# Performance work log

Hardware: AMD Instinct MI355X
Metric: run time of the kernel (lower is better)

The kernel has to match this reference:

```python
import jax, jax.numpy as jnp
import numpy as np

B, L, H, E = 4, 2048, 16, 64  # batch, seq, heads, head_dim (S=L, D=E)


def setup_inputs() -> dict:
    key = jax.random.key(0)
    kq, kk, kv = jax.random.split(key, 3)
    queries = jax.random.normal(kq, (B, L, H, E), dtype=jnp.float32)
    keys = jax.random.normal(kk, (B, L, H, E), dtype=jnp.float32)
    values = jax.random.normal(kv, (B, L, H, E), dtype=jnp.float32)
    return {"queries": queries, "keys": keys, "values": values}


def reference(queries, keys, values):
    Bq, Lq, Hq, Eq = queries.shape
    scale = 1.0 / float(np.sqrt(Eq))
    # scores: [B, H, L, S]
    scores = jnp.einsum('blhe,bshe->bhls', queries, keys)
    # causal mask: forbid attending to future positions (strict upper triangle)
    causal = jnp.triu(jnp.ones((Lq, Lq), dtype=bool), k=1)
    scores = jnp.where(causal[None, None, :, :], -jnp.inf, scores)
    A = jax.nn.softmax(scale * scores, axis=-1)  # dropout p=0 -> identity
    V = jnp.einsum('bhls,bshd->blhd', A, values)  # [B, L, H, D]
    return V
```

## Files before the change

### kernel.cpp

```cpp
#include <hip/hip_runtime.h>
#include <hip/hip_bf16.h>

typedef short bs8 __attribute__((ext_vector_type(8)));
typedef short bs4 __attribute__((ext_vector_type(4)));
typedef float f32x4 __attribute__((ext_vector_type(4)));
typedef float f32x16 __attribute__((ext_vector_type(16)));
typedef int i32x4 __attribute__((ext_vector_type(4)));

#define B_ 4
#define L_ 2048
#define H_ 16
#define E_ 64
#define KT_ 64
#define KSTR 72
#define SCSTR 68
#define NEG_INF (-1e30f)
#define SCALE_LOG2E (0.125f * 1.44269504088896340736f)

__device__ __forceinline__ short bf16of(float x) {
  __hip_bfloat16 h = __float2bfloat16(x);
  return *reinterpret_cast<short*>(&h);
}

__global__ __launch_bounds__(256) void prep(const float* __restrict__ K,
                                            const float* __restrict__ V,
                                            short* __restrict__ Kb,
                                            short* __restrict__ Vt) {
  __shared__ unsigned int lt[64 * 35];
  const int tid = threadIdx.x;
  if (blockIdx.x < 1024) {
    size_t base = (size_t)blockIdx.x * 256 + tid;
#pragma unroll
    for (int i = 0; i < 8; ++i) {
      size_t g = base + (size_t)i * 262144;
      int e4 = g & 15;
      int h  = (g >> 4) & 15;
      int s  = (g >> 8) & 2047;
      int b  = (int)(g >> 19);
      float4 v = *(const float4*)(K + g * 4);
      bs4 o;
      o.x = bf16of(v.x); o.y = bf16of(v.y); o.z = bf16of(v.z); o.w = bf16of(v.w);
      *(bs4*)(Kb + (((size_t)(b * 16 + h) * L_ + s) * E_ + e4 * 4)) = o;
    }
  } else {
    int vb = blockIdx.x - 1024;
    int st = vb & 31, bh = vb >> 5;
    int b = bh >> 4, h = bh & 15;
    int s0 = st * 64;
#pragma unroll
    for (int i = 0; i < 2; ++i) {
      int idx = i * 256 + tid;
      int sp = idx >> 4;
      int e4 = idx & 15;
      const float* p0 = V + (((size_t)b * L_ + s0 + 2 * sp) * H_ + h) * E_ + e4 * 4;
      float4 v0 = *(const float4*)p0;
      float4 v1 = *(const float4*)(p0 + H_ * E_);
      unsigned u;
      u = (unsigned short)bf16of(v0.x) | ((unsigned)(unsigned short)bf16of(v1.x) << 16);
      lt[(e4 * 4 + 0) * 35 + sp] = u;
      u = (unsigned short)bf16of(v0.y) | ((unsigned)(unsigned short)bf16of(v1.y) << 16);
      lt[(e4 * 4 + 1) * 35 + sp] = u;
      u = (unsigned short)bf16of(v0.z) | ((unsigned)(unsigned short)bf16of(v1.z) << 16);
      lt[(e4 * 4 + 2) * 35 + sp] = u;
      u = (unsigned short)bf16of(v0.w) | ((unsigned)(unsigned short)bf16of(v1.w) << 16);
      lt[(e4 * 4 + 3) * 35 + sp] = u;
    }
    __syncthreads();
#pragma unroll
    for (int i = 0; i < 2; ++i) {
      int idx = i * 256 + tid;
      int e  = idx >> 3;
      int s8 = idx & 7;
      uint4 o;
      o.x = lt[e * 35 + s8 * 4 + 0];
      o.y = lt[e * 35 + s8 * 4 + 1];
      o.z = lt[e * 35 + s8 * 4 + 2];
      o.w = lt[e * 35 + s8 * 4 + 3];
      *(uint4*)(Vt + ((size_t)bh * E_ + e) * L_ + s0 + 8 * s8) = o;
    }
  }
}

__global__ __launch_bounds__(256, 4) void flash_fwd(const float* __restrict__ Q,
                                                    const short* __restrict__ Kb,
                                                    const short* __restrict__ Vt,
                                                    float* __restrict__ O) {
  const int id  = blockIdx.x;
  const int xcd = id & 7;
  const int j   = id >> 3;
  const int bh  = xcd * 8 + (j >> 4);
  const int p   = j & 15;
  const int b = bh >> 4, h = bh & 15;
  const int tid = threadIdx.x;
  const int w = tid >> 6;
  const int g = w >> 1;
  const int s = w & 1;
  const int lane = tid & 63;
  const int l32 = lane & 31;
  const int hh  = lane >> 5;
  const int h8  = hh * 8;

  __shared__ __align__(16) char smem[18432];
  short* ldsK = (short*)smem;
  short* ldsV = (short*)(smem + KT_ * KSTR * 2);
  float* scb  = (float*)smem;

  const short* KbBase = Kb + (size_t)bh * L_ * E_;
  const short* VtBase = Vt + (size_t)bh * E_ * L_;

  const int sr = tid >> 3;
  const int sc8 = (tid & 7) * 8;

  for (int phase = 0; phase < 2; ++phase) {
    const int qt  = phase ? (31 - p) : p;
    const int q0w = qt * 64 + 32 * s;
    const int nkt = qt + 1;

    bs8 aQ[4];
    {
      const float* qp = Q + (((size_t)b * L_ + q0w + l32) * H_ + h) * E_ + h8;
#pragma unroll
      for (int ks = 0; ks < 4; ++ks) {
        float4 f0 = *(const float4*)(qp + ks * 16);
        float4 f1 = *(const float4*)(qp + ks * 16 + 4);
        bs8 a;
        a[0] = bf16of(f0.x * SCALE_LOG2E); a[1] = bf16of(f0.y * SCALE_LOG2E);
        a[2] = bf16of(f0.z * SCALE_LOG2E); a[3] = bf16of(f0.w * SCALE_LOG2E);
        a[4] = bf16of(f1.x * SCALE_LOG2E); a[5] = bf16of(f1.y * SCALE_LOG2E);
        a[6] = bf16of(f1.z * SCALE_LOG2E); a[7] = bf16of(f1.w * SCALE_LOG2E);
        aQ[ks] = a;
      }
    }

    f32x16 accO[2];
#pragma unroll
    for (int d = 0; d < 2; ++d)
#pragma unroll
      for (int r = 0; r < 16; ++r) accO[d][r] = 0.f;
    float accL = 0.f;

    bs8 pfK[2], pfV[2];
#pragma unroll
    for (int i = 0; i < 2; ++i) {
      pfK[i] = *(const bs8*)(KbBase + (size_t)(sr + 32 * i) * E_ + sc8);
      pfV[i] = *(const bs8*)(VtBase + (size_t)(sr + 32 * i) * L_ + sc8);
    }

    for (int kt = 0; kt < nkt; ++kt) {
      const int k0 = kt * KT_;
      __syncthreads();
#pragma unroll
      for (int i = 0; i < 2; ++i) {
        *(bs8*)&ldsK[(sr + 32 * i) * KSTR + sc8] = pfK[i];
        *(bs8*)&ldsV[(sr + 32 * i) * KSTR + sc8] = pfV[i];
      }
      if (kt + 1 < nkt) {
        const int kn = k0 + KT_;
#pragma unroll
        for (int i = 0; i < 2; ++i) {
          pfK[i] = *(const bs8*)(KbBase + (size_t)(kn + sr + 32 * i) * E_ + sc8);
          pfV[i] = *(const bs8*)(VtBase + (size_t)(sr + 32 * i) * L_ + kn + sc8);
        }
      }
      __syncthreads();

      const int kb = k0 + 32 * g;
      if (kb <= q0w + 31) {
        const bool diag = (kb + 31 > q0w);

        f32x16 cc;
#pragma unroll
        for (int r = 0; r < 16; ++r) cc[r] = 0.f;
#pragma unroll
        for (int ks = 0; ks < 4; ++ks) {
          bs8 aK = *(const bs8*)&ldsK[(32 * g + l32) * KSTR + ks * 16 + h8];
          cc = __builtin_amdgcn_mfma_f32_32x32x16_bf16(aK, aQ[ks], cc, 0, 0, 0);
        }
        if (diag) {
          const int qcol = q0w + l32;
#pragma unroll
          for (int r = 0; r < 16; ++r) {
            const int key = kb + ((r & 3) + 8 * (r >> 2) + 4 * hh);
            if (key > qcol) cc[r] = NEG_INF;
          }
        }
        float pv[16];
#pragma unroll
        for (int r = 0; r < 16; ++r) pv[r] = exp2f(cc[r]);
        accL += ((((pv[0] + pv[1]) + (pv[2] + pv[3])) + ((pv[4] + pv[5]) + (pv[6] + pv[7]))) +
                 (((pv[8] + pv[9]) + (pv[10] + pv[11])) + ((pv[12] + pv[13]) + (pv[14] + pv[15]))));
        unsigned pk[8];
#pragma unroll
        for (int i = 0; i < 8; ++i)
          pk[i] = (unsigned)(unsigned short)bf16of(pv[2 * i]) |
                  ((unsigned)(unsigned short)bf16of(pv[2 * i + 1]) << 16);
        unsigned w0 = pk[0], w2 = pk[2];
        asm("v_permlane32_swap_b32 %0, %1" : "+v"(w0), "+v"(w2));
        unsigned w1 = pk[1], w3 = pk[3];
        asm("v_permlane32_swap_b32 %0, %1" : "+v"(w1), "+v"(w3));
        unsigned w4 = pk[4], w6 = pk[6];
        asm("v_permlane32_swap_b32 %0, %1" : "+v"(w4), "+v"(w6));
        unsigned w5 = pk[5], w7 = pk[7];
        asm("v_permlane32_swap_b32 %0, %1" : "+v"(w5), "+v"(w7));
        i32x4 f0 = {(int)w0, (int)w1, (int)w2, (int)w3};
        i32x4 f1 = {(int)w4, (int)w5, (int)w6, (int)w7};
        bs8 pB0 = *(bs8*)&f0;
        bs8 pB1 = *(bs8*)&f1;

#pragma unroll
        for (int dsub = 0; dsub < 2; ++dsub) {
          bs8 aV0 = *(const bs8*)&ldsV[(dsub * 32 + l32) * KSTR + 32 * g + h8];
          bs8 aV1 = *(const bs8*)&ldsV[(dsub * 32 + l32) * KSTR + 32 * g + 16 + h8];
          accO[dsub] = __builtin_amdgcn_mfma_f32_32x32x16_bf16(aV0, pB0, accO[dsub], 0, 0, 0);
          accO[dsub] = __builtin_amdgcn_mfma_f32_32x32x16_bf16(aV1, pB1, accO[dsub], 0, 0, 0);
        }
      }
    }

    const float Lf = accL + __shfl_xor(accL, 32, 64);
    __syncthreads();
    float* scbO = scb + s * (32 * SCSTR);
    float* scbL = scb + 2 * (32 * SCSTR) + s * 32;
    if (g == 1) {
#pragma unroll
      for (int dsub = 0; dsub < 2; ++dsub)
#pragma unroll
        for (int q4 = 0; q4 < 4; ++q4) {
          f32x4 vv = {accO[dsub][4 * q4 + 0], accO[dsub][4 * q4 + 1],
                      accO[dsub][4 * q4 + 2], accO[dsub][4 * q4 + 3]};
          *(f32x4*)&scbO[(size_t)l32 * SCSTR + dsub * 32 + 8 * q4 + 4 * hh] = vv;
        }
      if (hh == 0) scbL[l32] = Lf;
    }
    __syncthreads();
    if (g == 0) {
      const float inv = 1.f / (Lf + scbL[l32]);
#pragma unroll
      for (int dsub = 0; dsub < 2; ++dsub)
#pragma unroll
        for (int q4 = 0; q4 < 4; ++q4) {
          float* ptr = &scbO[(size_t)l32 * SCSTR + dsub * 32 + 8 * q4 + 4 * hh];
          f32x4 ov = *(const f32x4*)ptr;
          f32x4 vv = {(accO[dsub][4 * q4 + 0] + ov.x) * inv,
                      (accO[dsub][4 * q4 + 1] + ov.y) * inv,
                      (accO[dsub][4 * q4 + 2] + ov.z) * inv,
                      (accO[dsub][4 * q4 + 3] + ov.w) * inv};
          *(f32x4*)ptr = vv;
        }
#pragma unroll
      for (int jj = 0; jj < 8; ++jj) {
        const int qq = jj * 4 + (lane >> 4);
        const int d0 = (lane & 15) * 4;
        f32x4 ov = *(const f32x4*)&scbO[(size_t)qq * SCSTR + d0];
        float* op = O + (((size_t)b * L_ + qt * 64 + 32 * s + qq) * H_ + h) * E_ + d0;
        *(f32x4*)op = ov;
      }
    }
  }
}

extern "C" void kernel_launch(void* const* d_in, const int* in_sizes, int n_in,
                              void* d_out, int out_size, void* d_ws, size_t ws_size,
                              hipStream_t stream) {
  (void)in_sizes; (void)n_in; (void)out_size; (void)ws_size;
  const float* Q = (const float*)d_in[0];
  const float* K = (const float*)d_in[1];
  const float* V = (const float*)d_in[2];
  float* Out = (float*)d_out;
  short* Kb = (short*)d_ws;
  short* Vt = Kb + (size_t)B_ * H_ * L_ * E_;

  prep<<<1024 + 2048, 256, 0, stream>>>(K, V, Kb, Vt);
  flash_fwd<<<1024, 256, 0, stream>>>(Q, Kb, Vt, Out);
}
```

Measured before the change: 201.3 us.

## Load K/V MFMA operands directly from global, drop LDS staging and barriers

Removes the LDS double-buffered staging of K and V tiles and the two per-iteration __syncthreads, so each wave reads its MFMA operands for K and transposed V straight from global memory (L2/cache). Waves now proceed independently and skip masked tiles with continue. It also switches to the fast exp2 builtin and packs bf16 pairs with v_cvt_pk_bf16_f32. The cost is that the two wave groups sharing a K/V tile each fetch it from global, giving less coalesced 16-byte accesses and more cache traffic.

```diff
diff --git a/kernel.cpp b/kernel.cpp
--- a/kernel.cpp
+++ b/kernel.cpp
@@ -12,7 +12,6 @@
 #define H_ 16
 #define E_ 64
 #define KT_ 64
-#define KSTR 72
 #define SCSTR 68
 #define NEG_INF (-1e30f)
 #define SCALE_LOG2E (0.125f * 1.44269504088896340736f)
@@ -100,16 +99,10 @@
   const int hh  = lane >> 5;
   const int h8  = hh * 8;
 
-  __shared__ __align__(16) char smem[18432];
-  short* ldsK = (short*)smem;
-  short* ldsV = (short*)(smem + KT_ * KSTR * 2);
-  float* scb  = (float*)smem;
+  __shared__ float scb[2 * 32 * SCSTR + 64];
 
   const short* KbBase = Kb + (size_t)bh * L_ * E_;
   const short* VtBase = Vt + (size_t)bh * E_ * L_;
-
-  const int sr = tid >> 3;
-  const int sc8 = (tid & 7) * 8;
 
   for (int phase = 0; phase < 2; ++phase) {
     const int qt  = phase ? (31 - p) : p;
@@ -139,81 +132,58 @@
       for (int r = 0; r < 16; ++r) accO[d][r] = 0.f;
     float accL = 0.f;
 
-    bs8 pfK[2], pfV[2];
-#pragma unroll
-    for (int i = 0; i < 2; ++i) {
-      pfK[i] = *(const bs8*)(KbBase + (size_t)(sr + 32 * i) * E_ + sc8);
-      pfV[i] = *(const bs8*)(VtBase + (size_t)(sr + 32 * i) * L_ + sc8);
-    }
-
     for (int kt = 0; kt < nkt; ++kt) {
-      const int k0 = kt * KT_;
-      __syncthreads();
-#pragma unroll
-      for (int i = 0; i < 2; ++i) {
-        *(bs8*)&ldsK[(sr + 32 * i) * KSTR + sc8] = pfK[i];
-        *(bs8*)&ldsV[(sr + 32 * i) * KSTR + sc8] = pfV[i];
-      }
-      if (kt + 1 < nkt) {
-        const int kn = k0 + KT_;
-#pragma unroll
-        for (int i = 0; i < 2; ++i) {
-          pfK[i] = *(const bs8*)(KbBase + (size_t)(kn + sr + 32 * i) * E_ + sc8);
-          pfV[i] = *(const bs8*)(VtBase + (size_t)(sr + 32 * i) * L_ + kn + sc8);
+      const int kb = kt * KT_ + 32 * g;
+      if (kb > q0w + 31) continue;
+      const bool diag = (kb + 31 > q0w);
+
+      f32x16 cc;
+#pragma unroll
+      for (int r = 0; r < 16; ++r) cc[r] = 0.f;
+      const short* kp = KbBase + (size_t)(kb + l32) * E_ + h8;
+#pragma unroll
+      for (int ks = 0; ks < 4; ++ks) {
+        bs8 aK = *(const bs8*)(kp + ks * 16);
+        cc = __builtin_amdgcn_mfma_f32_32x32x16_bf16(aK, aQ[ks], cc, 0, 0, 0);
+      }
+      if (diag) {
+        const int qcol = q0w + l32;
+#pragma unroll
+        for (int r = 0; r < 16; ++r) {
+          const int key = kb + ((r & 3) + 8 * (r >> 2) + 4 * hh);
+          if (key > qcol) cc[r] = NEG_INF;
         }
       }
-      __syncthreads();
-
-      const int kb = k0 + 32 * g;
-      if (kb <= q0w + 31) {
-        const bool diag = (kb + 31 > q0w);
-
-        f32x16 cc;
-#pragma unroll
-        for (int r = 0; r < 16; ++r) cc[r] = 0.f;
-#pragma unroll
-        for (int ks = 0; ks < 4; ++ks) {
-          bs8 aK = *(const bs8*)&ldsK[(32 * g + l32) * KSTR + ks * 16 + h8];
-          cc = __builtin_amdgcn_mfma_f32_32x32x16_bf16(aK, aQ[ks], cc, 0, 0, 0);
-        }
-        if (diag) {
-          const int qcol = q0w + l32;
-#pragma unroll
-          for (int r = 0; r < 16; ++r) {
-            const int key = kb + ((r & 3) + 8 * (r >> 2) + 4 * hh);
-            if (key > qcol) cc[r] = NEG_INF;
-          }
-        }
-        float pv[16];
-#pragma unroll
-        for (int r = 0; r < 16; ++r) pv[r] = exp2f(cc[r]);
-        accL += ((((pv[0] + pv[1]) + (pv[2] + pv[3])) + ((pv[4] + pv[5]) + (pv[6] + pv[7]))) +
-                 (((pv[8] + pv[9]) + (pv[10] + pv[11])) + ((pv[12] + pv[13]) + (pv[14] + pv[15]))));
-        unsigned pk[8];
-#pragma unroll
-        for (int i = 0; i < 8; ++i)
-          pk[i] = (unsigned)(unsigned short)bf16of(pv[2 * i]) |
-                  ((unsigned)(unsigned short)bf16of(pv[2 * i + 1]) << 16);
-        unsigned w0 = pk[0], w2 = pk[2];
-        asm("v_permlane32_swap_b32 %0, %1" : "+v"(w0), "+v"(w2));
-        unsigned w1 = pk[1], w3 = pk[3];
-        asm("v_permlane32_swap_b32 %0, %1" : "+v"(w1), "+v"(w3));
-        unsigned w4 = pk[4], w6 = pk[6];
-        asm("v_permlane32_swap_b32 %0, %1" : "+v"(w4), "+v"(w6));
-        unsigned w5 = pk[5], w7 = pk[7];
-        asm("v_permlane32_swap_b32 %0, %1" : "+v"(w5), "+v"(w7));
-        i32x4 f0 = {(int)w0, (int)w1, (int)w2, (int)w3};
-        i32x4 f1 = {(int)w4, (int)w5, (int)w6, (int)w7};
-        bs8 pB0 = *(bs8*)&f0;
-        bs8 pB1 = *(bs8*)&f1;
-
-#pragma unroll
-        for (int dsub = 0; dsub < 2; ++dsub) {
-          bs8 aV0 = *(const bs8*)&ldsV[(dsub * 32 + l32) * KSTR + 32 * g + h8];
-          bs8 aV1 = *(const bs8*)&ldsV[(dsub * 32 + l32) * KSTR + 32 * g + 16 + h8];
-          accO[dsub] = __builtin_amdgcn_mfma_f32_32x32x16_bf16(aV0, pB0, accO[dsub], 0, 0, 0);
-          accO[dsub] = __builtin_amdgcn_mfma_f32_32x32x16_bf16(aV1, pB1, accO[dsub], 0, 0, 0);
-        }
+      float pv[16];
+#pragma unroll
+      for (int r = 0; r < 16; ++r) pv[r] = __builtin_amdgcn_exp2f(cc[r]);
+      accL += ((((pv[0] + pv[1]) + (pv[2] + pv[3])) + ((pv[4] + pv[5]) + (pv[6] + pv[7]))) +
+               (((pv[8] + pv[9]) + (pv[10] + pv[11])) + ((pv[12] + pv[13]) + (pv[14] + pv[15]))));
+      unsigned pk[8];
+#pragma unroll
+      for (int i = 0; i < 8; ++i)
+        asm("v_cvt_pk_bf16_f32 %0, %1, %2"
+            : "=v"(pk[i]) : "v"(pv[2 * i]), "v"(pv[2 * i + 1]));
+      unsigned w0 = pk[0], w2 = pk[2];
+      asm("v_permlane32_swap_b32 %0, %1" : "+v"(w0), "+v"(w2));
+      unsigned w1 = pk[1], w3 = pk[3];
+      asm("v_permlane32_swap_b32 %0, %1" : "+v"(w1), "+v"(w3));
+      unsigned w4 = pk[4], w6 = pk[6];
+      asm("v_permlane32_swap_b32 %0, %1" : "+v"(w4), "+v"(w6));
+      unsigned w5 = pk[5], w7 = pk[7];
+      asm("v_permlane32_swap_b32 %0, %1" : "+v"(w5), "+v"(w7));
+      i32x4 f0 = {(int)w0, (int)w1, (int)w2, (int)w3};
+      i32x4 f1 = {(int)w4, (int)w5, (int)w6, (int)w7};
+      bs8 pB0 = *(bs8*)&f0;
+      bs8 pB1 = *(bs8*)&f1;
+
+#pragma unroll
+      for (int dsub = 0; dsub < 2; ++dsub) {
+        const short* vp = VtBase + (size_t)(dsub * 32 + l32) * L_ + kb + h8;
+        bs8 aV0 = *(const bs8*)(vp);
+        bs8 aV1 = *(const bs8*)(vp + 16);
+        accO[dsub] = __builtin_amdgcn_mfma_f32_32x32x16_bf16(aV0, pB0, accO[dsub], 0, 0, 0);
+        accO[dsub] = __builtin_amdgcn_mfma_f32_32x32x16_bf16(aV1, pB1, accO[dsub], 0, 0, 0);
       }
     }
 
```

Result: slower. 252.0 us (+25.2%).
